# Optimization experiments

Measured on AMD Instinct MI355X. Metric: run time of the kernel, lower is better.

The kernel has to match this reference:

```python
import jax, jax.numpy as jnp
import numpy as np

B, S, D = 64, 4096, 256

def setup_inputs() -> dict:
    key = jax.random.key(0)
    k1, k2, k3 = jax.random.split(key, 3)
    x = jax.random.normal(k1, (B, S, D), dtype=jnp.float32)
    # glorot-scale params
    W = jax.random.normal(k2, (D, D), dtype=jnp.float32) * (1.0 / np.sqrt(D))
    b = jnp.zeros((D,), dtype=jnp.float32)
    u = jax.random.normal(k3, (D, 1), dtype=jnp.float32) * (1.0 / np.sqrt(D))
    return {"x": x, "W": W, "b": b, "u": u}

def reference(x, W, b, u):
    # uit: [B,S,D] = tanh(x @ W + b)
    uit = jnp.tanh(jnp.einsum('bsd,de->bse', x, W) + b)
    # score: [B,S]
    score = jnp.einsum('bsd,d->bs', uit, u[:, 0])
    weights = jax.nn.softmax(score, axis=1)          # [B,S]
    context = jnp.einsum('bs,bsd->bd', weights, x)   # [B,D]
    return (context, weights)
```

## Files before the change

kernel.cpp:

```cpp
#include <hip/hip_runtime.h>
#include <hip/hip_bf16.h>
#include <cstdint>
#include <cstddef>

#define B_ 64
#define S_ 4096
#define D_ 256
#define BM 64
#define BK 64
#define NBLK (B_ * S_ / BM)
#define BLKS_PER_B (S_ / BM)

typedef __attribute__((ext_vector_type(8))) short short8;
typedef __attribute__((ext_vector_type(4))) float f32x4;
typedef __attribute__((ext_vector_type(4))) float f4;

__device__ __forceinline__ short f2bf(float f) {
  union { float f; uint32_t u; } v; v.f = f;
  uint32_t r = v.u + 0x7FFFu + ((v.u >> 16) & 1u);
  return (short)(r >> 16);
}

__device__ __forceinline__ float fast_tanh(float z) {
  return 1.0f - 2.0f / (__expf(2.0f * z) + 1.0f);
}

__device__ __forceinline__ void gload_lds16(const short* g, short* l) {
  __builtin_amdgcn_global_load_lds(
      (const __attribute__((address_space(1))) int*)(g),
      (__attribute__((address_space(3))) int*)(l), 16, 0, 0);
}

__global__ void k_pack(const float* __restrict__ W, short* __restrict__ wt) {
  __shared__ float tile[64][65];
  int t = blockIdx.x, ti = t >> 2, tj = t & 3;
  int tid = threadIdx.x;
#pragma unroll
  for (int i = 0; i < 16; ++i) {
    int idx = i * 256 + tid;
    int r = idx >> 6, c = idx & 63;
    tile[c][r] = W[(ti * 64 + r) * 256 + tj * 64 + c];
  }
  __syncthreads();
#pragma unroll
  for (int i = 0; i < 16; ++i) {
    int idx = i * 256 + tid;
    int r = idx >> 6, c = idx & 63;
    wt[(tj * 64 + r) * 256 + ti * 64 + c] = f2bf(tile[r][c]);
  }
}

__global__ __launch_bounds__(256, 3)
void k_scores(const float* __restrict__ x, const short* __restrict__ wt,
              const float* __restrict__ bias, const float* __restrict__ u,
              float* __restrict__ ws_scores, float* __restrict__ ws_m,
              float* __restrict__ ws_l, float* __restrict__ ws_c) {
  __shared__ __align__(16) short lsB[D_ * BK];
  __shared__ float score_lds[BM];
  __shared__ float e_lds[BM];
  __shared__ float red_lds[1];

  const int tid = threadIdx.x;
  const int bid = blockIdx.x;
  const int m0 = bid * BM;
  const int lane = tid & 63;
  const int wv = tid >> 6;
  const int cl = lane & 15;
  const int gr = lane >> 4;

  const int st_n  = ((0 * 256 + tid) >> 3);
  (void)st_n;

  f32x4 acc[16];
#pragma unroll
  for (int j = 0; j < 16; ++j) acc[j] = (f32x4){0.f, 0.f, 0.f, 0.f};

#pragma unroll
  for (int i = 0; i < 8; ++i) {
    int idx = i * 256 + tid;
    int n = idx >> 3, c8 = idx & 7;
    gload_lds16(wt + n * 256 + ((c8 ^ (n & 7)) << 3), &lsB[idx * 8]);
  }

  const float* xrow = x + (size_t)(m0 + wv * 16 + cl) * D_;
  const int roff = cl * 64;
  const int sw0 = ((0 + gr) ^ (cl & 7)) << 3;
  const int sw1 = ((4 + gr) ^ (cl & 7)) << 3;

  for (int kc = 0; kc < 4; ++kc) {
    f4 a00 = *(const f4*)(xrow + kc * 64 + gr * 8);
    f4 a01 = *(const f4*)(xrow + kc * 64 + gr * 8 + 4);
    f4 a10 = *(const f4*)(xrow + kc * 64 + 32 + gr * 8);
    f4 a11 = *(const f4*)(xrow + kc * 64 + 32 + gr * 8 + 4);
    __syncthreads();

    short8 af0, af1;
    af0[0] = f2bf(a00[0]); af0[1] = f2bf(a00[1]); af0[2] = f2bf(a00[2]); af0[3] = f2bf(a00[3]);
    af0[4] = f2bf(a01[0]); af0[5] = f2bf(a01[1]); af0[6] = f2bf(a01[2]); af0[7] = f2bf(a01[3]);
    af1[0] = f2bf(a10[0]); af1[1] = f2bf(a10[1]); af1[2] = f2bf(a10[2]); af1[3] = f2bf(a10[3]);
    af1[4] = f2bf(a11[0]); af1[5] = f2bf(a11[1]); af1[6] = f2bf(a11[2]); af1[7] = f2bf(a11[3]);

#pragma unroll
    for (int nf = 0; nf < 16; ++nf) {
      short8 b0 = *(const short8*)&lsB[nf * 1024 + roff + sw0];
      acc[nf] = __builtin_amdgcn_mfma_f32_16x16x32_bf16(af0, b0, acc[nf], 0, 0, 0);
      short8 b1 = *(const short8*)&lsB[nf * 1024 + roff + sw1];
      acc[nf] = __builtin_amdgcn_mfma_f32_16x16x32_bf16(af1, b1, acc[nf], 0, 0, 0);
    }
    __syncthreads();
    if (kc < 3) {
#pragma unroll
      for (int i = 0; i < 8; ++i) {
        int idx = i * 256 + tid;
        int n = idx >> 3, c8 = idx & 7;
        gload_lds16(wt + n * 256 + (kc + 1) * 64 + ((c8 ^ (n & 7)) << 3), &lsB[idx * 8]);
      }
    }
  }

  float bv[16], uv[16];
#pragma unroll
  for (int nf = 0; nf < 16; ++nf) {
    bv[nf] = bias[nf * 16 + cl];
    uv[nf] = u[nf * 16 + cl];
  }
  float p0 = 0.f, p1 = 0.f, p2 = 0.f, p3 = 0.f;
#pragma unroll
  for (int nf = 0; nf < 16; ++nf) {
    p0 += fast_tanh(acc[nf][0] + bv[nf]) * uv[nf];
    p1 += fast_tanh(acc[nf][1] + bv[nf]) * uv[nf];
    p2 += fast_tanh(acc[nf][2] + bv[nf]) * uv[nf];
    p3 += fast_tanh(acc[nf][3] + bv[nf]) * uv[nf];
  }
#pragma unroll
  for (int m = 1; m < 16; m <<= 1) {
    p0 += __shfl_xor(p0, m);
    p1 += __shfl_xor(p1, m);
    p2 += __shfl_xor(p2, m);
    p3 += __shfl_xor(p3, m);
  }
  if (cl == 0) {
    int r = wv * 16 + gr * 4;
    score_lds[r + 0] = p0;
    score_lds[r + 1] = p1;
    score_lds[r + 2] = p2;
    score_lds[r + 3] = p3;
    ws_scores[m0 + r + 0] = p0;
    ws_scores[m0 + r + 1] = p1;
    ws_scores[m0 + r + 2] = p2;
    ws_scores[m0 + r + 3] = p3;
  }
  __syncthreads();
  if (tid < 64) {
    float v = score_lds[tid];
#pragma unroll
    for (int m = 32; m >= 1; m >>= 1) v = fmaxf(v, __shfl_xor(v, m));
    if (tid == 0) red_lds[0] = v;
  }
  __syncthreads();
  float mb = red_lds[0];
  if (tid < BM) e_lds[tid] = __expf(score_lds[tid] - mb);
  __syncthreads();
  if (tid < 64) {
    float v = e_lds[tid];
#pragma unroll
    for (int m = 32; m >= 1; m >>= 1) v += __shfl_xor(v, m);
    if (tid == 0) { ws_m[bid] = mb; ws_l[bid] = v; }
  }
  float cacc = 0.f;
  const float* xp = x + (size_t)m0 * D_ + tid;
#pragma unroll 4
  for (int s = 0; s < BM; ++s) cacc += e_lds[s] * xp[(size_t)s * D_];
  ws_c[bid * D_ + tid] = cacc;
}

__global__ void k_combine(const float* __restrict__ ws_m, const float* __restrict__ ws_l,
                          const float* __restrict__ ws_c, float* __restrict__ out_ctx,
                          float* __restrict__ ws_M, float* __restrict__ ws_L) {
  int b = blockIdx.x, d = threadIdx.x;
  float M = -1e30f;
#pragma unroll
  for (int i = 0; i < BLKS_PER_B; ++i) M = fmaxf(M, ws_m[b * BLKS_PER_B + i]);
  float L = 0.f, c = 0.f;
#pragma unroll 4
  for (int i = 0; i < BLKS_PER_B; ++i) {
    float f = __expf(ws_m[b * BLKS_PER_B + i] - M);
    L += ws_l[b * BLKS_PER_B + i] * f;
    c += ws_c[(b * BLKS_PER_B + i) * D_ + d] * f;
  }
  out_ctx[b * D_ + d] = c / L;
  if (d == 0) { ws_M[b] = M; ws_L[b] = L; }
}

__global__ void k_weights(const float* __restrict__ ws_scores, const float* __restrict__ ws_M,
                          const float* __restrict__ ws_L, float* __restrict__ out_w) {
  int idx = blockIdx.x * 256 + threadIdx.x;
  int b = idx >> 12;
  out_w[idx] = __expf(ws_scores[idx] - ws_M[b]) / ws_L[b];
}

extern "C" void kernel_launch(void* const* d_in, const int* in_sizes, int n_in,
                              void* d_out, int out_size, void* d_ws, size_t ws_size,
                              hipStream_t stream) {
  (void)in_sizes; (void)n_in; (void)out_size; (void)ws_size;
  const float* x    = (const float*)d_in[0];
  const float* W    = (const float*)d_in[1];
  const float* bias = (const float*)d_in[2];
  const float* u    = (const float*)d_in[3];
  float* out_ctx = (float*)d_out;
  float* out_w   = (float*)d_out + B_ * D_;

  char* ws = (char*)d_ws;
  short* wt        = (short*)(ws + 0);
  float* ws_scores = (float*)(ws + 131072);
  float* ws_m      = (float*)(ws + 1179648);
  float* ws_l      = (float*)(ws + 1196032);
  float* ws_c      = (float*)(ws + 1212416);
  float* ws_M      = (float*)(ws + 5406720);
  float* ws_L      = (float*)(ws + 5406976);

  hipLaunchKernelGGL(k_pack, dim3(16), dim3(256), 0, stream, W, wt);
  hipLaunchKernelGGL(k_scores, dim3(NBLK), dim3(256), 0, stream,
                     x, wt, bias, u, ws_scores, ws_m, ws_l, ws_c);
  hipLaunchKernelGGL(k_combine, dim3(B_), dim3(256), 0, stream,
                     ws_m, ws_l, ws_c, out_ctx, ws_M, ws_L);
  hipLaunchKernelGGL(k_weights, dim3(B_ * S_ / 256), dim3(256), 0, stream,
                     ws_scores, ws_M, ws_L, out_w);
}
```

Baseline: 117.8 us.

## Make score kernel persistent with register-resident W and double-buffered x tiles

Rewrites k_scores as a persistent kernel: 256 blocks of 1024 threads, each looping over 16 row tiles of 64. Each wave keeps its 32-column slice of packed W in registers, so W is no longer restaged into LDS for every tile. The next x tile is prefetched into registers and written as bf16 into a double-buffered, swizzled LDS tile. Scores are combined across 8 column-group waves through LDS, and the context sum is split four ways across threads. The cost is fewer, larger blocks (lower occupancy), more barriers per tile, and x rows still being re-read from global memory for the context sum.

```diff
diff --git a/kernel.cpp b/kernel.cpp
--- a/kernel.cpp
+++ b/kernel.cpp
@@ -7,8 +7,9 @@
 #define S_ 4096
 #define D_ 256
 #define BM 64
-#define BK 64
-#define NBLK (B_ * S_ / BM)
+#define TPB 1024
+#define TILES_PER_BLOCK 16
+#define GRID 256
 #define BLKS_PER_B (S_ / BM)
 
 typedef __attribute__((ext_vector_type(8))) short short8;
@@ -25,12 +26,6 @@
   return 1.0f - 2.0f / (__expf(2.0f * z) + 1.0f);
 }
 
-__device__ __forceinline__ void gload_lds16(const short* g, short* l) {
-  __builtin_amdgcn_global_load_lds(
-      (const __attribute__((address_space(1))) int*)(g),
-      (__attribute__((address_space(3))) int*)(l), 16, 0, 0);
-}
-
 __global__ void k_pack(const float* __restrict__ W, short* __restrict__ wt) {
   __shared__ float tile[64][65];
   int t = blockIdx.x, ti = t >> 2, tj = t & 3;
@@ -50,128 +45,157 @@
   }
 }
 
-__global__ __launch_bounds__(256, 3)
+__global__ __launch_bounds__(TPB)
 void k_scores(const float* __restrict__ x, const short* __restrict__ wt,
               const float* __restrict__ bias, const float* __restrict__ u,
               float* __restrict__ ws_scores, float* __restrict__ ws_m,
               float* __restrict__ ws_l, float* __restrict__ ws_c) {
-  __shared__ __align__(16) short lsB[D_ * BK];
-  __shared__ float score_lds[BM];
+  __shared__ __align__(16) short lsA[2][BM * D_];
+  __shared__ float score_part[BM][8];
   __shared__ float e_lds[BM];
-  __shared__ float red_lds[1];
-
-  const int tid = threadIdx.x;
-  const int bid = blockIdx.x;
-  const int m0 = bid * BM;
+  __shared__ float ctx_part[4][D_];
+
+  const int tid  = threadIdx.x;
   const int lane = tid & 63;
-  const int wv = tid >> 6;
-  const int cl = lane & 15;
-  const int gr = lane >> 4;
-
-  const int st_n  = ((0 * 256 + tid) >> 3);
-  (void)st_n;
-
-  f32x4 acc[16];
-#pragma unroll
-  for (int j = 0; j < 16; ++j) acc[j] = (f32x4){0.f, 0.f, 0.f, 0.f};
-
-#pragma unroll
-  for (int i = 0; i < 8; ++i) {
-    int idx = i * 256 + tid;
-    int n = idx >> 3, c8 = idx & 7;
-    gload_lds16(wt + n * 256 + ((c8 ^ (n & 7)) << 3), &lsB[idx * 8]);
-  }
-
-  const float* xrow = x + (size_t)(m0 + wv * 16 + cl) * D_;
-  const int roff = cl * 64;
-  const int sw0 = ((0 + gr) ^ (cl & 7)) << 3;
-  const int sw1 = ((4 + gr) ^ (cl & 7)) << 3;
-
-  for (int kc = 0; kc < 4; ++kc) {
-    f4 a00 = *(const f4*)(xrow + kc * 64 + gr * 8);
-    f4 a01 = *(const f4*)(xrow + kc * 64 + gr * 8 + 4);
-    f4 a10 = *(const f4*)(xrow + kc * 64 + 32 + gr * 8);
-    f4 a11 = *(const f4*)(xrow + kc * 64 + 32 + gr * 8 + 4);
-    __syncthreads();
-
-    short8 af0, af1;
-    af0[0] = f2bf(a00[0]); af0[1] = f2bf(a00[1]); af0[2] = f2bf(a00[2]); af0[3] = f2bf(a00[3]);
-    af0[4] = f2bf(a01[0]); af0[5] = f2bf(a01[1]); af0[6] = f2bf(a01[2]); af0[7] = f2bf(a01[3]);
-    af1[0] = f2bf(a10[0]); af1[1] = f2bf(a10[1]); af1[2] = f2bf(a10[2]); af1[3] = f2bf(a10[3]);
-    af1[4] = f2bf(a11[0]); af1[5] = f2bf(a11[1]); af1[6] = f2bf(a11[2]); af1[7] = f2bf(a11[3]);
-
-#pragma unroll
-    for (int nf = 0; nf < 16; ++nf) {
-      short8 b0 = *(const short8*)&lsB[nf * 1024 + roff + sw0];
-      acc[nf] = __builtin_amdgcn_mfma_f32_16x16x32_bf16(af0, b0, acc[nf], 0, 0, 0);
-      short8 b1 = *(const short8*)&lsB[nf * 1024 + roff + sw1];
-      acc[nf] = __builtin_amdgcn_mfma_f32_16x16x32_bf16(af1, b1, acc[nf], 0, 0, 0);
-    }
-    __syncthreads();
-    if (kc < 3) {
-#pragma unroll
-      for (int i = 0; i < 8; ++i) {
-        int idx = i * 256 + tid;
-        int n = idx >> 3, c8 = idx & 7;
-        gload_lds16(wt + n * 256 + (kc + 1) * 64 + ((c8 ^ (n & 7)) << 3), &lsB[idx * 8]);
+  const int wv   = tid >> 6;
+  const int cg   = wv & 7;
+  const int rg   = wv >> 3;
+  const int cl   = lane & 15;
+  const int gr   = lane >> 4;
+  const int swzr = (cl & 7) << 4;
+
+  short8 bfr0[8], bfr1[8];
+  {
+    const short* w0 = wt + (cg * 32 + cl) * D_ + gr * 8;
+    const short* w1 = w0 + 16 * D_;
+#pragma unroll
+    for (int kf = 0; kf < 8; ++kf) {
+      bfr0[kf] = *(const short8*)(w0 + kf * 32);
+      bfr1[kf] = *(const short8*)(w1 + kf * 32);
+    }
+  }
+  const float bv0 = bias[cg * 32 + cl], bv1 = bias[cg * 32 + 16 + cl];
+  const float uv0 = u[cg * 32 + cl],    uv1 = u[cg * 32 + 16 + cl];
+
+  const int block0 = blockIdx.x * (TILES_PER_BLOCK * BM);
+
+  const int sr = tid >> 4;
+  const int sc = (tid & 15) * 16;
+  const int swzw = (sr & 7) << 4;
+  const int wb0 = sr * 512 + ((sc * 2) ^ swzw);
+  const int wb1 = sr * 512 + ((sc * 2 + 16) ^ swzw);
+
+  {
+    const float* xs = x + ((size_t)block0 + sr) * D_ + sc;
+    f4 g0 = *(const f4*)(xs + 0), g1 = *(const f4*)(xs + 4);
+    f4 g2 = *(const f4*)(xs + 8), g3 = *(const f4*)(xs + 12);
+    short8 s0, s1;
+    s0[0]=f2bf(g0[0]); s0[1]=f2bf(g0[1]); s0[2]=f2bf(g0[2]); s0[3]=f2bf(g0[3]);
+    s0[4]=f2bf(g1[0]); s0[5]=f2bf(g1[1]); s0[6]=f2bf(g1[2]); s0[7]=f2bf(g1[3]);
+    s1[0]=f2bf(g2[0]); s1[1]=f2bf(g2[1]); s1[2]=f2bf(g2[2]); s1[3]=f2bf(g2[3]);
+    s1[4]=f2bf(g3[0]); s1[5]=f2bf(g3[1]); s1[6]=f2bf(g3[2]); s1[7]=f2bf(g3[3]);
+    char* b0 = (char*)&lsA[0][0];
+    *(short8*)(b0 + wb0) = s0;
+    *(short8*)(b0 + wb1) = s1;
+  }
+
+  const int r0byte = (rg * 32 + cl) * 512;
+  const int r1byte = r0byte + 16 * 512;
+  const int gb = gr * 16;
+
+  for (int t = 0; t < TILES_PER_BLOCK; ++t) {
+    const int t0 = block0 + t * BM;
+    const int tile_idx = blockIdx.x * TILES_PER_BLOCK + t;
+
+    f4 n0, n1, n2, n3;
+    if (t < TILES_PER_BLOCK - 1) {
+      const float* xn = x + ((size_t)t0 + BM + sr) * D_ + sc;
+      n0 = *(const f4*)(xn + 0); n1 = *(const f4*)(xn + 4);
+      n2 = *(const f4*)(xn + 8); n3 = *(const f4*)(xn + 12);
+    }
+
+    __syncthreads();
+
+    const char* A = (const char*)&lsA[t & 1][0];
+    f32x4 acc00 = {0.f,0.f,0.f,0.f}, acc01 = {0.f,0.f,0.f,0.f};
+    f32x4 acc10 = {0.f,0.f,0.f,0.f}, acc11 = {0.f,0.f,0.f,0.f};
+#pragma unroll
+    for (int kf = 0; kf < 8; ++kf) {
+      const int co = (kf * 64 + gb) ^ swzr;
+      short8 a0 = *(const short8*)(A + r0byte + co);
+      short8 a1 = *(const short8*)(A + r1byte + co);
+      acc00 = __builtin_amdgcn_mfma_f32_16x16x32_bf16(a0, bfr0[kf], acc00, 0, 0, 0);
+      acc01 = __builtin_amdgcn_mfma_f32_16x16x32_bf16(a0, bfr1[kf], acc01, 0, 0, 0);
+      acc10 = __builtin_amdgcn_mfma_f32_16x16x32_bf16(a1, bfr0[kf], acc10, 0, 0, 0);
+      acc11 = __builtin_amdgcn_mfma_f32_16x16x32_bf16(a1, bfr1[kf], acc11, 0, 0, 0);
+    }
+
+    float q0[4], q1[4];
+#pragma unroll
+    for (int j = 0; j < 4; ++j) {
+      q0[j] = fast_tanh(acc00[j] + bv0) * uv0 + fast_tanh(acc01[j] + bv1) * uv1;
+      q1[j] = fast_tanh(acc10[j] + bv0) * uv0 + fast_tanh(acc11[j] + bv1) * uv1;
+    }
+#pragma unroll
+    for (int m = 1; m < 16; m <<= 1) {
+#pragma unroll
+      for (int j = 0; j < 4; ++j) {
+        q0[j] += __shfl_xor(q0[j], m);
+        q1[j] += __shfl_xor(q1[j], m);
       }
     }
-  }
-
-  float bv[16], uv[16];
-#pragma unroll
-  for (int nf = 0; nf < 16; ++nf) {
-    bv[nf] = bias[nf * 16 + cl];
-    uv[nf] = u[nf * 16 + cl];
-  }
-  float p0 = 0.f, p1 = 0.f, p2 = 0.f, p3 = 0.f;
-#pragma unroll
-  for (int nf = 0; nf < 16; ++nf) {
-    p0 += fast_tanh(acc[nf][0] + bv[nf]) * uv[nf];
-    p1 += fast_tanh(acc[nf][1] + bv[nf]) * uv[nf];
-    p2 += fast_tanh(acc[nf][2] + bv[nf]) * uv[nf];
-    p3 += fast_tanh(acc[nf][3] + bv[nf]) * uv[nf];
-  }
-#pragma unroll
-  for (int m = 1; m < 16; m <<= 1) {
-    p0 += __shfl_xor(p0, m);
-    p1 += __shfl_xor(p1, m);
-    p2 += __shfl_xor(p2, m);
-    p3 += __shfl_xor(p3, m);
-  }
-  if (cl == 0) {
-    int r = wv * 16 + gr * 4;
-    score_lds[r + 0] = p0;
-    score_lds[r + 1] = p1;
-    score_lds[r + 2] = p2;
-    score_lds[r + 3] = p3;
-    ws_scores[m0 + r + 0] = p0;
-    ws_scores[m0 + r + 1] = p1;
-    ws_scores[m0 + r + 2] = p2;
-    ws_scores[m0 + r + 3] = p3;
-  }
-  __syncthreads();
-  if (tid < 64) {
-    float v = score_lds[tid];
-#pragma unroll
-    for (int m = 32; m >= 1; m >>= 1) v = fmaxf(v, __shfl_xor(v, m));
-    if (tid == 0) red_lds[0] = v;
-  }
-  __syncthreads();
-  float mb = red_lds[0];
-  if (tid < BM) e_lds[tid] = __expf(score_lds[tid] - mb);
-  __syncthreads();
-  if (tid < 64) {
-    float v = e_lds[tid];
-#pragma unroll
-    for (int m = 32; m >= 1; m >>= 1) v += __shfl_xor(v, m);
-    if (tid == 0) { ws_m[bid] = mb; ws_l[bid] = v; }
-  }
-  float cacc = 0.f;
-  const float* xp = x + (size_t)m0 * D_ + tid;
-#pragma unroll 4
-  for (int s = 0; s < BM; ++s) cacc += e_lds[s] * xp[(size_t)s * D_];
-  ws_c[bid * D_ + tid] = cacc;
+    if (cl == 0) {
+      const int rb = rg * 32 + gr * 4;
+#pragma unroll
+      for (int j = 0; j < 4; ++j) {
+        score_part[rb + j][cg]      = q0[j];
+        score_part[rb + 16 + j][cg] = q1[j];
+      }
+    }
+    __syncthreads();
+
+    if (tid < 64) {
+      float s = score_part[tid][0] + score_part[tid][1] + score_part[tid][2] +
+                score_part[tid][3] + score_part[tid][4] + score_part[tid][5] +
+                score_part[tid][6] + score_part[tid][7];
+      float mx = s;
+#pragma unroll
+      for (int off = 32; off >= 1; off >>= 1) mx = fmaxf(mx, __shfl_xor(mx, off));
+      float e = __expf(s - mx);
+      e_lds[tid] = e;
+      float l = e;
+#pragma unroll
+      for (int off = 32; off >= 1; off >>= 1) l += __shfl_xor(l, off);
+      ws_scores[t0 + tid] = s;
+      if (tid == 0) { ws_m[tile_idx] = mx; ws_l[tile_idx] = l; }
+    }
+    __syncthreads();
+
+    {
+      const int qq = tid >> 8, d = tid & 255;
+      const float* xp = x + ((size_t)t0 + qq * 16) * D_ + d;
+      float c = 0.f;
+#pragma unroll
+      for (int s2 = 0; s2 < 16; ++s2)
+        c = fmaf(e_lds[qq * 16 + s2], xp[(size_t)s2 * D_], c);
+      ctx_part[qq][d] = c;
+    }
+    __syncthreads();
+    if (tid < 256)
+      ws_c[(size_t)tile_idx * D_ + tid] =
+          ctx_part[0][tid] + ctx_part[1][tid] + ctx_part[2][tid] + ctx_part[3][tid];
+
+    if (t < TILES_PER_BLOCK - 1) {
+      short8 s0, s1;
+      s0[0]=f2bf(n0[0]); s0[1]=f2bf(n0[1]); s0[2]=f2bf(n0[2]); s0[3]=f2bf(n0[3]);
+      s0[4]=f2bf(n1[0]); s0[5]=f2bf(n1[1]); s0[6]=f2bf(n1[2]); s0[7]=f2bf(n1[3]);
+      s1[0]=f2bf(n2[0]); s1[1]=f2bf(n2[1]); s1[2]=f2bf(n2[2]); s1[3]=f2bf(n2[3]);
+      s1[4]=f2bf(n3[0]); s1[5]=f2bf(n3[1]); s1[6]=f2bf(n3[2]); s1[7]=f2bf(n3[3]);
+      char* bn = (char*)&lsA[(t + 1) & 1][0];
+      *(short8*)(bn + wb0) = s0;
+      *(short8*)(bn + wb1) = s1;
+    }
+  }
 }
 
 __global__ void k_combine(const float* __restrict__ ws_m, const float* __restrict__ ws_l,
@@ -186,7 +210,7 @@
   for (int i = 0; i < BLKS_PER_B; ++i) {
     float f = __expf(ws_m[b * BLKS_PER_B + i] - M);
     L += ws_l[b * BLKS_PER_B + i] * f;
-    c += ws_c[(b * BLKS_PER_B + i) * D_ + d] * f;
+    c += ws_c[(size_t)(b * BLKS_PER_B + i) * D_ + d] * f;
   }
   out_ctx[b * D_ + d] = c / L;
   if (d == 0) { ws_M[b] = M; ws_L[b] = L; }
@@ -220,7 +244,7 @@
   float* ws_L      = (float*)(ws + 5406976);
 
   hipLaunchKernelGGL(k_pack, dim3(16), dim3(256), 0, stream, W, wt);
-  hipLaunchKernelGGL(k_scores, dim3(NBLK), dim3(256), 0, stream,
+  hipLaunchKernelGGL(k_scores, dim3(GRID), dim3(TPB), 0, stream,
                      x, wt, bias, u, ws_scores, ws_m, ws_l, ws_c);
   hipLaunchKernelGGL(k_combine, dim3(B_), dim3(256), 0, stream,
                      ws_m, ws_l, ws_c, out_ctx, ws_M, ws_L);
```

Result: slower. 236.0 us (+100.3%).

## Double rows per block in score kernel to reuse each LDS W fragment twice

Applied to the files above, without the earlier changes.

Each wave now handles two 16-row strips, so every B fragment read from LDS feeds two MFMAs. Block size along S goes from 64 to 128, which halves the number of blocks and the per-block W loads and partial context writes. Bias and u are staged once into LDS. The cost is twice the accumulator registers, with launch bounds lowered to two blocks per CU, which may reduce occupancy and latency hiding for the x loads.

```diff
diff --git a/kernel.cpp b/kernel.cpp
--- a/kernel.cpp
+++ b/kernel.cpp
@@ -6,7 +6,7 @@
 #define B_ 64
 #define S_ 4096
 #define D_ 256
-#define BM 64
+#define BM 128
 #define BK 64
 #define NBLK (B_ * S_ / BM)
 #define BLKS_PER_B (S_ / BM)
@@ -50,30 +50,31 @@
   }
 }
 
-__global__ __launch_bounds__(256, 3)
+__global__ __launch_bounds__(256, 2)
 void k_scores(const float* __restrict__ x, const short* __restrict__ wt,
               const float* __restrict__ bias, const float* __restrict__ u,
               float* __restrict__ ws_scores, float* __restrict__ ws_m,
               float* __restrict__ ws_l, float* __restrict__ ws_c) {
   __shared__ __align__(16) short lsB[D_ * BK];
+  __shared__ __align__(8) float bu[D_ * 2];
   __shared__ float score_lds[BM];
   __shared__ float e_lds[BM];
   __shared__ float red_lds[1];
 
-  const int tid = threadIdx.x;
-  const int bid = blockIdx.x;
-  const int m0 = bid * BM;
+  const int tid  = threadIdx.x;
+  const int bid  = blockIdx.x;
+  const int m0   = bid * BM;
   const int lane = tid & 63;
-  const int wv = tid >> 6;
-  const int cl = lane & 15;
-  const int gr = lane >> 4;
-
-  const int st_n  = ((0 * 256 + tid) >> 3);
-  (void)st_n;
-
-  f32x4 acc[16];
-#pragma unroll
-  for (int j = 0; j < 16; ++j) acc[j] = (f32x4){0.f, 0.f, 0.f, 0.f};
+  const int wv   = tid >> 6;
+  const int cl   = lane & 15;
+  const int gr   = lane >> 4;
+
+  f32x4 acc0[16], acc1[16];
+#pragma unroll
+  for (int j = 0; j < 16; ++j) {
+    acc0[j] = (f32x4){0.f, 0.f, 0.f, 0.f};
+    acc1[j] = (f32x4){0.f, 0.f, 0.f, 0.f};
+  }
 
 #pragma unroll
   for (int i = 0; i < 8; ++i) {
@@ -81,31 +82,46 @@
     int n = idx >> 3, c8 = idx & 7;
     gload_lds16(wt + n * 256 + ((c8 ^ (n & 7)) << 3), &lsB[idx * 8]);
   }
-
-  const float* xrow = x + (size_t)(m0 + wv * 16 + cl) * D_;
-  const int roff = cl * 64;
+  if (tid < D_) {
+    bu[tid * 2]     = bias[tid];
+    bu[tid * 2 + 1] = u[tid];
+  }
+
+  const float* xrow0 = x + (size_t)(m0 + wv * 32 + cl) * D_;
+  const float* xrow1 = xrow0 + 16 * D_;
+  const int rbase = cl * 64;
   const int sw0 = ((0 + gr) ^ (cl & 7)) << 3;
   const int sw1 = ((4 + gr) ^ (cl & 7)) << 3;
 
   for (int kc = 0; kc < 4; ++kc) {
-    f4 a00 = *(const f4*)(xrow + kc * 64 + gr * 8);
-    f4 a01 = *(const f4*)(xrow + kc * 64 + gr * 8 + 4);
-    f4 a10 = *(const f4*)(xrow + kc * 64 + 32 + gr * 8);
-    f4 a11 = *(const f4*)(xrow + kc * 64 + 32 + gr * 8 + 4);
+    f4 a00 = *(const f4*)(xrow0 + kc * 64 + gr * 8);
+    f4 a01 = *(const f4*)(xrow0 + kc * 64 + gr * 8 + 4);
+    f4 a02 = *(const f4*)(xrow0 + kc * 64 + 32 + gr * 8);
+    f4 a03 = *(const f4*)(xrow0 + kc * 64 + 32 + gr * 8 + 4);
+    f4 a10 = *(const f4*)(xrow1 + kc * 64 + gr * 8);
+    f4 a11 = *(const f4*)(xrow1 + kc * 64 + gr * 8 + 4);
+    f4 a12 = *(const f4*)(xrow1 + kc * 64 + 32 + gr * 8);
+    f4 a13 = *(const f4*)(xrow1 + kc * 64 + 32 + gr * 8 + 4);
     __syncthreads();
 
-    short8 af0, af1;
-    af0[0] = f2bf(a00[0]); af0[1] = f2bf(a00[1]); af0[2] = f2bf(a00[2]); af0[3] = f2bf(a00[3]);
-    af0[4] = f2bf(a01[0]); af0[5] = f2bf(a01[1]); af0[6] = f2bf(a01[2]); af0[7] = f2bf(a01[3]);
-    af1[0] = f2bf(a10[0]); af1[1] = f2bf(a10[1]); af1[2] = f2bf(a10[2]); af1[3] = f2bf(a10[3]);
-    af1[4] = f2bf(a11[0]); af1[5] = f2bf(a11[1]); af1[6] = f2bf(a11[2]); af1[7] = f2bf(a11[3]);
+    short8 f0k0, f0k1, f1k0, f1k1;
+    f0k0[0]=f2bf(a00[0]); f0k0[1]=f2bf(a00[1]); f0k0[2]=f2bf(a00[2]); f0k0[3]=f2bf(a00[3]);
+    f0k0[4]=f2bf(a01[0]); f0k0[5]=f2bf(a01[1]); f0k0[6]=f2bf(a01[2]); f0k0[7]=f2bf(a01[3]);
+    f0k1[0]=f2bf(a02[0]); f0k1[1]=f2bf(a02[1]); f0k1[2]=f2bf(a02[2]); f0k1[3]=f2bf(a02[3]);
+    f0k1[4]=f2bf(a03[0]); f0k1[5]=f2bf(a03[1]); f0k1[6]=f2bf(a03[2]); f0k1[7]=f2bf(a03[3]);
+    f1k0[0]=f2bf(a10[0]); f1k0[1]=f2bf(a10[1]); f1k0[2]=f2bf(a10[2]); f1k0[3]=f2bf(a10[3]);
+    f1k0[4]=f2bf(a11[0]); f1k0[5]=f2bf(a11[1]); f1k0[6]=f2bf(a11[2]); f1k0[7]=f2bf(a11[3]);
+    f1k1[0]=f2bf(a12[0]); f1k1[1]=f2bf(a12[1]); f1k1[2]=f2bf(a12[2]); f1k1[3]=f2bf(a12[3]);
+    f1k1[4]=f2bf(a13[0]); f1k1[5]=f2bf(a13[1]); f1k1[6]=f2bf(a13[2]); f1k1[7]=f2bf(a13[3]);
 
 #pragma unroll
     for (int nf = 0; nf < 16; ++nf) {
-      short8 b0 = *(const short8*)&lsB[nf * 1024 + roff + sw0];
-      acc[nf] = __builtin_amdgcn_mfma_f32_16x16x32_bf16(af0, b0, acc[nf], 0, 0, 0);
-      short8 b1 = *(const short8*)&lsB[nf * 1024 + roff + sw1];
-      acc[nf] = __builtin_amdgcn_mfma_f32_16x16x32_bf16(af1, b1, acc[nf], 0, 0, 0);
+      short8 b0 = *(const short8*)&lsB[nf * 1024 + rbase + sw0];
+      acc0[nf] = __builtin_amdgcn_mfma_f32_16x16x32_bf16(f0k0, b0, acc0[nf], 0, 0, 0);
+      acc1[nf] = __builtin_amdgcn_mfma_f32_16x16x32_bf16(f1k0, b0, acc1[nf], 0, 0, 0);
+      short8 b1 = *(const short8*)&lsB[nf * 1024 + rbase + sw1];
+      acc0[nf] = __builtin_amdgcn_mfma_f32_16x16x32_bf16(f0k1, b1, acc0[nf], 0, 0, 0);
+      acc1[nf] = __builtin_amdgcn_mfma_f32_16x16x32_bf16(f1k1, b1, acc1[nf], 0, 0, 0);
     }
     __syncthreads();
     if (kc < 3) {
@@ -118,41 +134,41 @@
     }
   }
 
-  float bv[16], uv[16];
-#pragma unroll
-  for (int nf = 0; nf < 16; ++nf) {
-    bv[nf] = bias[nf * 16 + cl];
-    uv[nf] = u[nf * 16 + cl];
-  }
-  float p0 = 0.f, p1 = 0.f, p2 = 0.f, p3 = 0.f;
-#pragma unroll
-  for (int nf = 0; nf < 16; ++nf) {
-    p0 += fast_tanh(acc[nf][0] + bv[nf]) * uv[nf];
-    p1 += fast_tanh(acc[nf][1] + bv[nf]) * uv[nf];
-    p2 += fast_tanh(acc[nf][2] + bv[nf]) * uv[nf];
-    p3 += fast_tanh(acc[nf][3] + bv[nf]) * uv[nf];
-  }
-#pragma unroll
-  for (int m = 1; m < 16; m <<= 1) {
-    p0 += __shfl_xor(p0, m);
-    p1 += __shfl_xor(p1, m);
-    p2 += __shfl_xor(p2, m);
-    p3 += __shfl_xor(p3, m);
-  }
-  if (cl == 0) {
-    int r = wv * 16 + gr * 4;
-    score_lds[r + 0] = p0;
-    score_lds[r + 1] = p1;
-    score_lds[r + 2] = p2;
-    score_lds[r + 3] = p3;
-    ws_scores[m0 + r + 0] = p0;
-    ws_scores[m0 + r + 1] = p1;
-    ws_scores[m0 + r + 2] = p2;
-    ws_scores[m0 + r + 3] = p3;
+#pragma unroll
+  for (int mi = 0; mi < 2; ++mi) {
+    float p0 = 0.f, p1 = 0.f, p2 = 0.f, p3 = 0.f;
+#pragma unroll
+    for (int nf = 0; nf < 16; ++nf) {
+      float bb = bu[(nf * 16 + cl) * 2];
+      float uu = bu[(nf * 16 + cl) * 2 + 1];
+      f32x4 av = (mi == 0) ? acc0[nf] : acc1[nf];
+      p0 += fast_tanh(av[0] + bb) * uu;
+      p1 += fast_tanh(av[1] + bb) * uu;
+      p2 += fast_tanh(av[2] + bb) * uu;
+      p3 += fast_tanh(av[3] + bb) * uu;
+    }
+#pragma unroll
+    for (int m = 1; m < 16; m <<= 1) {
+      p0 += __shfl_xor(p0, m);
+      p1 += __shfl_xor(p1, m);
+      p2 += __shfl_xor(p2, m);
+      p3 += __shfl_xor(p3, m);
+    }
+    if (cl == 0) {
+      int r = wv * 32 + mi * 16 + gr * 4;
+      score_lds[r + 0] = p0;
+      score_lds[r + 1] = p1;
+      score_lds[r + 2] = p2;
+      score_lds[r + 3] = p3;
+      ws_scores[m0 + r + 0] = p0;
+      ws_scores[m0 + r + 1] = p1;
+      ws_scores[m0 + r + 2] = p2;
+      ws_scores[m0 + r + 3] = p3;
+    }
   }
   __syncthreads();
   if (tid < 64) {
-    float v = score_lds[tid];
+    float v = fmaxf(score_lds[tid], score_lds[tid + 64]);
 #pragma unroll
     for (int m = 32; m >= 1; m >>= 1) v = fmaxf(v, __shfl_xor(v, m));
     if (tid == 0) red_lds[0] = v;
@@ -162,7 +178,7 @@
   if (tid < BM) e_lds[tid] = __expf(score_lds[tid] - mb);
   __syncthreads();
   if (tid < 64) {
-    float v = e_lds[tid];
+    float v = e_lds[tid] + e_lds[tid + 64];
 #pragma unroll
     for (int m = 32; m >= 1; m >>= 1) v += __shfl_xor(v, m);
     if (tid == 0) { ws_m[bid] = mb; ws_l[bid] = v; }
@@ -178,7 +194,7 @@
                           const float* __restrict__ ws_c, float* __restrict__ out_ctx,
                           float* __restrict__ ws_M, float* __restrict__ ws_L) {
   int b = blockIdx.x, d = threadIdx.x;
-  float M = -1e30f;
+  float M = -3.4e38f;
 #pragma unroll
   for (int i = 0; i < BLKS_PER_B; ++i) M = fmaxf(M, ws_m[b * BLKS_PER_B + i]);
   float L = 0.f, c = 0.f;
@@ -186,7 +202,7 @@
   for (int i = 0; i < BLKS_PER_B; ++i) {
     float f = __expf(ws_m[b * BLKS_PER_B + i] - M);
     L += ws_l[b * BLKS_PER_B + i] * f;
-    c += ws_c[(b * BLKS_PER_B + i) * D_ + d] * f;
+    c += ws_c[(size_t)(b * BLKS_PER_B + i) * D_ + d] * f;
   }
   out_ctx[b * D_ + d] = c / L;
   if (d == 0) { ws_M[b] = M; ws_L[b] = L; }
@@ -214,10 +230,10 @@
   short* wt        = (short*)(ws + 0);
   float* ws_scores = (float*)(ws + 131072);
   float* ws_m      = (float*)(ws + 1179648);
-  float* ws_l      = (float*)(ws + 1196032);
-  float* ws_c      = (float*)(ws + 1212416);
-  float* ws_M      = (float*)(ws + 5406720);
-  float* ws_L      = (float*)(ws + 5406976);
+  float* ws_l      = (float*)(ws + 1187840);
+  float* ws_c      = (float*)(ws + 1196032);
+  float* ws_M      = (float*)(ws + 3293184);
+  float* ws_L      = (float*)(ws + 3293440);
 
   hipLaunchKernelGGL(k_pack, dim3(16), dim3(256), 0, stream, W, wt);
   hipLaunchKernelGGL(k_scores, dim3(NBLK), dim3(256), 0, stream,
```

Result: slower. 140.1 us (+18.9%).

## Double-buffer W tiles in LDS with explicit vmcnt waits and prefetched x fragments

Applied to the files above, without the earlier changes.

Rewrites the score GEMM main loop into an 8-step pipeline with K=32 chunks. Two LDS buffers for the packed W tile let the next chunk stream in while the current one feeds MFMAs, and x fragments are prefetched two steps ahead, with manual s_waitcnt and s_barrier control. The change also stages bias and u in LDS, uses a hardware reciprocal in tanh, and runs k_pack with 1024 threads. It drops the XOR swizzle on the LDS layout, which risks bank conflicts, and the hand-tuned wait counts are fragile.

```diff
diff --git a/kernel.cpp b/kernel.cpp
--- a/kernel.cpp
+++ b/kernel.cpp
@@ -7,7 +7,7 @@
 #define S_ 4096
 #define D_ 256
 #define BM 64
-#define BK 64
+#define BK 32
 #define NBLK (B_ * S_ / BM)
 #define BLKS_PER_B (S_ / BM)
 
@@ -22,7 +22,7 @@
 }
 
 __device__ __forceinline__ float fast_tanh(float z) {
-  return 1.0f - 2.0f / (__expf(2.0f * z) + 1.0f);
+  return 1.0f - 2.0f * __builtin_amdgcn_rcpf(__expf(2.0f * z) + 1.0f);
 }
 
 __device__ __forceinline__ void gload_lds16(const short* g, short* l) {
@@ -36,101 +36,109 @@
   int t = blockIdx.x, ti = t >> 2, tj = t & 3;
   int tid = threadIdx.x;
 #pragma unroll
-  for (int i = 0; i < 16; ++i) {
-    int idx = i * 256 + tid;
+  for (int i = 0; i < 4; ++i) {
+    int idx = i * 1024 + tid;
     int r = idx >> 6, c = idx & 63;
     tile[c][r] = W[(ti * 64 + r) * 256 + tj * 64 + c];
   }
   __syncthreads();
 #pragma unroll
-  for (int i = 0; i < 16; ++i) {
-    int idx = i * 256 + tid;
+  for (int i = 0; i < 4; ++i) {
+    int idx = i * 1024 + tid;
     int r = idx >> 6, c = idx & 63;
     wt[(tj * 64 + r) * 256 + ti * 64 + c] = f2bf(tile[r][c]);
   }
 }
+
+#define WAITV(N) asm volatile("s_waitcnt vmcnt(" #N ")" ::: "memory")
+#define FENCE()  asm volatile("" ::: "memory")
+
+#define STAGE(BUF, KC)                                                        \
+  {                                                                           \
+    _Pragma("unroll")                                                         \
+    for (int i_ = 0; i_ < 4; ++i_) {                                          \
+      int c_ = i_ * 256 + tid;                                                \
+      int n_ = c_ >> 2, ko_ = (c_ & 3) * 8;                                   \
+      gload_lds16(wt + n_ * 256 + (KC) * 32 + ko_, &lsB[BUF][c_ * 8]);        \
+    }                                                                         \
+  }
+
+#define ITER(KC, VM, SCA, SCB, SLA, SLB, DOSTAGE, DOLOAD)                     \
+  {                                                                           \
+    if (DOSTAGE) STAGE(((KC) + 1) & 1, (KC) + 1);                             \
+    if (DOLOAD) {                                                             \
+      SLA = *(const f4*)(xrow + ((KC) + 2) * 32);                             \
+      SLB = *(const f4*)(xrow + ((KC) + 2) * 32 + 4);                         \
+    }                                                                         \
+    WAITV(VM);                                                                \
+    asm volatile("s_waitcnt lgkmcnt(0)" ::: "memory");                        \
+    __builtin_amdgcn_sched_barrier(0);                                        \
+    __builtin_amdgcn_s_barrier();                                             \
+    FENCE();                                                                  \
+    short8 fr_;                                                               \
+    fr_[0]=f2bf(SCA[0]); fr_[1]=f2bf(SCA[1]); fr_[2]=f2bf(SCA[2]); fr_[3]=f2bf(SCA[3]); \
+    fr_[4]=f2bf(SCB[0]); fr_[5]=f2bf(SCB[1]); fr_[6]=f2bf(SCB[2]); fr_[7]=f2bf(SCB[3]); \
+    _Pragma("unroll")                                                         \
+    for (int nf_ = 0; nf_ < 16; ++nf_) {                                      \
+      short8 bfr_ = *(const short8*)&lsB[(KC) & 1][(nf_ * 16 + cl) * 32 + gr * 8]; \
+      acc[nf_] = __builtin_amdgcn_mfma_f32_16x16x32_bf16(fr_, bfr_, acc[nf_], 0, 0, 0); \
+    }                                                                         \
+    FENCE();                                                                  \
+    __builtin_amdgcn_s_barrier();                                             \
+    FENCE();                                                                  \
+  }
 
 __global__ __launch_bounds__(256, 3)
 void k_scores(const float* __restrict__ x, const short* __restrict__ wt,
               const float* __restrict__ bias, const float* __restrict__ u,
               float* __restrict__ ws_scores, float* __restrict__ ws_m,
               float* __restrict__ ws_l, float* __restrict__ ws_c) {
-  __shared__ __align__(16) short lsB[D_ * BK];
+  __shared__ __align__(16) short lsB[2][D_ * BK];
+  __shared__ __align__(8) float bu[D_ * 2];
   __shared__ float score_lds[BM];
   __shared__ float e_lds[BM];
   __shared__ float red_lds[1];
 
-  const int tid = threadIdx.x;
-  const int bid = blockIdx.x;
-  const int m0 = bid * BM;
+  const int tid  = threadIdx.x;
+  const int bid  = blockIdx.x;
+  const int m0   = bid * BM;
   const int lane = tid & 63;
-  const int wv = tid >> 6;
-  const int cl = lane & 15;
-  const int gr = lane >> 4;
-
-  const int st_n  = ((0 * 256 + tid) >> 3);
-  (void)st_n;
+  const int wv   = tid >> 6;
+  const int cl   = lane & 15;
+  const int gr   = lane >> 4;
+
+  bu[tid * 2]     = bias[tid];
+  bu[tid * 2 + 1] = u[tid];
 
   f32x4 acc[16];
 #pragma unroll
   for (int j = 0; j < 16; ++j) acc[j] = (f32x4){0.f, 0.f, 0.f, 0.f};
 
-#pragma unroll
-  for (int i = 0; i < 8; ++i) {
-    int idx = i * 256 + tid;
-    int n = idx >> 3, c8 = idx & 7;
-    gload_lds16(wt + n * 256 + ((c8 ^ (n & 7)) << 3), &lsB[idx * 8]);
-  }
-
-  const float* xrow = x + (size_t)(m0 + wv * 16 + cl) * D_;
-  const int roff = cl * 64;
-  const int sw0 = ((0 + gr) ^ (cl & 7)) << 3;
-  const int sw1 = ((4 + gr) ^ (cl & 7)) << 3;
-
-  for (int kc = 0; kc < 4; ++kc) {
-    f4 a00 = *(const f4*)(xrow + kc * 64 + gr * 8);
-    f4 a01 = *(const f4*)(xrow + kc * 64 + gr * 8 + 4);
-    f4 a10 = *(const f4*)(xrow + kc * 64 + 32 + gr * 8);
-    f4 a11 = *(const f4*)(xrow + kc * 64 + 32 + gr * 8 + 4);
-    __syncthreads();
-
-    short8 af0, af1;
-    af0[0] = f2bf(a00[0]); af0[1] = f2bf(a00[1]); af0[2] = f2bf(a00[2]); af0[3] = f2bf(a00[3]);
-    af0[4] = f2bf(a01[0]); af0[5] = f2bf(a01[1]); af0[6] = f2bf(a01[2]); af0[7] = f2bf(a01[3]);
-    af1[0] = f2bf(a10[0]); af1[1] = f2bf(a10[1]); af1[2] = f2bf(a10[2]); af1[3] = f2bf(a10[3]);
-    af1[4] = f2bf(a11[0]); af1[5] = f2bf(a11[1]); af1[6] = f2bf(a11[2]); af1[7] = f2bf(a11[3]);
-
-#pragma unroll
-    for (int nf = 0; nf < 16; ++nf) {
-      short8 b0 = *(const short8*)&lsB[nf * 1024 + roff + sw0];
-      acc[nf] = __builtin_amdgcn_mfma_f32_16x16x32_bf16(af0, b0, acc[nf], 0, 0, 0);
-      short8 b1 = *(const short8*)&lsB[nf * 1024 + roff + sw1];
-      acc[nf] = __builtin_amdgcn_mfma_f32_16x16x32_bf16(af1, b1, acc[nf], 0, 0, 0);
-    }
-    __syncthreads();
-    if (kc < 3) {
-#pragma unroll
-      for (int i = 0; i < 8; ++i) {
-        int idx = i * 256 + tid;
-        int n = idx >> 3, c8 = idx & 7;
-        gload_lds16(wt + n * 256 + (kc + 1) * 64 + ((c8 ^ (n & 7)) << 3), &lsB[idx * 8]);
-      }
-    }
-  }
-
-  float bv[16], uv[16];
+  const float* xrow = x + (size_t)(m0 + wv * 16 + cl) * D_ + gr * 8;
+
+  f4 s0a, s0b, s1a, s1b, s2a, s2b;
+  s0a = *(const f4*)(xrow);       s0b = *(const f4*)(xrow + 4);
+  STAGE(0, 0);
+  s1a = *(const f4*)(xrow + 32);  s1b = *(const f4*)(xrow + 36);
+
+  ITER(0, 8, s0a, s0b, s2a, s2b, 1, 1)
+  ITER(1, 8, s1a, s1b, s0a, s0b, 1, 1)
+  ITER(2, 8, s2a, s2b, s1a, s1b, 1, 1)
+  ITER(3, 8, s0a, s0b, s2a, s2b, 1, 1)
+  ITER(4, 8, s1a, s1b, s0a, s0b, 1, 1)
+  ITER(5, 8, s2a, s2b, s1a, s1b, 1, 1)
+  ITER(6, 6, s0a, s0b, s0a, s0b, 1, 0)
+  ITER(7, 0, s1a, s1b, s0a, s0b, 0, 0)
+
+  float p0 = 0.f, p1 = 0.f, p2 = 0.f, p3 = 0.f;
 #pragma unroll
   for (int nf = 0; nf < 16; ++nf) {
-    bv[nf] = bias[nf * 16 + cl];
-    uv[nf] = u[nf * 16 + cl];
-  }
-  float p0 = 0.f, p1 = 0.f, p2 = 0.f, p3 = 0.f;
-#pragma unroll
-  for (int nf = 0; nf < 16; ++nf) {
-    p0 += fast_tanh(acc[nf][0] + bv[nf]) * uv[nf];
-    p1 += fast_tanh(acc[nf][1] + bv[nf]) * uv[nf];
-    p2 += fast_tanh(acc[nf][2] + bv[nf]) * uv[nf];
-    p3 += fast_tanh(acc[nf][3] + bv[nf]) * uv[nf];
+    float bb = bu[(nf * 16 + cl) * 2];
+    float uu = bu[(nf * 16 + cl) * 2 + 1];
+    p0 += fast_tanh(acc[nf][0] + bb) * uu;
+    p1 += fast_tanh(acc[nf][1] + bb) * uu;
+    p2 += fast_tanh(acc[nf][2] + bb) * uu;
+    p3 += fast_tanh(acc[nf][3] + bb) * uu;
   }
 #pragma unroll
   for (int m = 1; m < 16; m <<= 1) {
@@ -178,7 +186,7 @@
                           const float* __restrict__ ws_c, float* __restrict__ out_ctx,
                           float* __restrict__ ws_M, float* __restrict__ ws_L) {
   int b = blockIdx.x, d = threadIdx.x;
-  float M = -1e30f;
+  float M = -3.4e38f;
 #pragma unroll
   for (int i = 0; i < BLKS_PER_B; ++i) M = fmaxf(M, ws_m[b * BLKS_PER_B + i]);
   float L = 0.f, c = 0.f;
@@ -186,7 +194,7 @@
   for (int i = 0; i < BLKS_PER_B; ++i) {
     float f = __expf(ws_m[b * BLKS_PER_B + i] - M);
     L += ws_l[b * BLKS_PER_B + i] * f;
-    c += ws_c[(b * BLKS_PER_B + i) * D_ + d] * f;
+    c += ws_c[(size_t)(b * BLKS_PER_B + i) * D_ + d] * f;
   }
   out_ctx[b * D_ + d] = c / L;
   if (d == 0) { ws_M[b] = M; ws_L[b] = L; }
@@ -219,7 +227,7 @@
   float* ws_M      = (float*)(ws + 5406720);
   float* ws_L      = (float*)(ws + 5406976);
 
-  hipLaunchKernelGGL(k_pack, dim3(16), dim3(256), 0, stream, W, wt);
+  hipLaunchKernelGGL(k_pack, dim3(16), dim3(1024), 0, stream, W, wt);
   hipLaunchKernelGGL(k_scores, dim3(NBLK), dim3(256), 0, stream,
                      x, wt, bias, u, ws_scores, ws_m, ws_l, ws_c);
   hipLaunchKernelGGL(k_combine, dim3(B_), dim3(256), 0, stream,
```

After: 115.9 us. No clear change (-1.6%).
